# Kernel optimization log

Measured on AMD Instinct MI355X. Metric: run time of the kernel, lower is better.

## Reference

```python
import jax, jax.numpy as jnp
import numpy as np

N, C_IN, C_OUT, W_DIM, H, W = 16, 512, 512, 512, 64, 64

def setup_inputs() -> dict:
    key = jax.random.key(0)
    ks = jax.random.split(key, 6)
    return {
        "x": jax.random.normal(ks[0], (N, C_IN, H, W), dtype=jnp.float32),
        "w": jax.random.normal(ks[1], (N, W_DIM), dtype=jnp.float32),
        "noise": jax.random.normal(ks[2], (N, 1, H, W), dtype=jnp.float32),
        "affine_w": jax.random.normal(ks[3], (C_IN, W_DIM), dtype=jnp.float32) * (1.0 / np.sqrt(W_DIM)),
        "affine_b": jnp.ones((C_IN,), dtype=jnp.float32),  # bias_init=1.0
        "noise_strength": jnp.ones((), dtype=jnp.float32),
        "conv_w": jax.random.normal(ks[4], (C_OUT, C_IN, 3, 3), dtype=jnp.float32),
        "conv_b": jnp.zeros((C_OUT,), dtype=jnp.float32),
    }

def reference(x, w, noise, affine_w, affine_b, noise_strength, conv_w, conv_b):
    # affine: s = w @ affine_w.T + affine_b  (no activation)
    s = jnp.einsum('nd,cd->nc', w, affine_w) + affine_b  # [N, C_in]
    # Demodulated per-sample conv. Original builds w_n = W * s_n then demodulates;
    # since conv is linear in the weight's input-channel scale, this is equivalent to
    # scaling the input by s and the output by the demod factor d.
    w2 = jnp.sum(conv_w * conv_w, axis=(2, 3))  # [O, I]: sum over kernel taps
    d = jax.lax.rsqrt(jnp.einsum('ni,oi->no', s * s, w2) + 1e-8)  # [N, O]
    x_mod = x * s[:, :, None, None]
    y = jax.lax.conv_general_dilated(
        x_mod, conv_w, window_strides=(1, 1), padding='SAME',
        dimension_numbers=('NCHW', 'OIHW', 'NCHW'))  # [N, O, H, W]
    y = y * d[:, :, None, None] + conv_b[None, :, None, None]
    y = y + noise * noise_strength
    return jnp.where(y >= 0, y, 0.2 * y)  # LeakyReLU(0.2)
```

## Files before the change

kernel.cpp:

```cpp
#include <hip/hip_runtime.h>
#include <hip/hip_bf16.h>

typedef unsigned short u16;
typedef short bf16x8 __attribute__((ext_vector_type(8)));
typedef float f32x4 __attribute__((ext_vector_type(4)));

#define N_    16
#define CIN   512
#define COUT  512
#define WD    512
#define P_    4096
#define CC    (COUT * CIN)

#define OFF_S   0u
#define OFF_D   32768u
#define OFF_Z   65536u
#define OFF_WBT 131072u
#define OFF_XB  8388608u
#define WS_NEED (OFF_XB + 67108864u)

__device__ __forceinline__ u16 f2bf(float f) {
  union { float f; unsigned u; } a; a.f = f;
  unsigned r = a.u + 0x7fffu + ((a.u >> 16) & 1u);
  return (u16)(r >> 16);
}

__device__ __forceinline__ void gl_lds16(const u16* g, u16* l) {
  __builtin_amdgcn_global_load_lds(
      (const __attribute__((address_space(1))) void*)g,
      (__attribute__((address_space(3))) void*)l, 16, 0, 0);
}

__global__ void k_zero(float* z) { z[threadIdx.x] = 0.f; }

__global__ __launch_bounds__(256) void k_affine(const float* __restrict__ w,
                                                const float* __restrict__ aw,
                                                const float* __restrict__ ab,
                                                float* __restrict__ s) {
  int idx = blockIdx.x * 256 + threadIdx.x;
  int n = idx >> 9, c = idx & 511;
  const float4* wr = (const float4*)(w + (size_t)n * WD);
  const float4* ar = (const float4*)(aw + (size_t)c * WD);
  float acc = 0.f;
#pragma unroll 4
  for (int k = 0; k < WD / 4; ++k) {
    float4 a = wr[k], b = ar[k];
    acc += a.x * b.x + a.y * b.y + a.z * b.z + a.w * b.w;
  }
  s[idx] = acc + ab[c];
}

__global__ __launch_bounds__(256) void k_demod(const float* __restrict__ s,
                                               const float* __restrict__ cw,
                                               float* __restrict__ d) {
  __shared__ float w2[CIN];
  int o = blockIdx.x;
  const float* wr = cw + (size_t)o * CIN * 9;
  for (int i = threadIdx.x; i < CIN; i += 256) {
    float acc = 0.f;
#pragma unroll
    for (int t = 0; t < 9; ++t) { float v = wr[i * 9 + t]; acc += v * v; }
    w2[i] = acc;
  }
  __syncthreads();
  int wave = threadIdx.x >> 6, lane = threadIdx.x & 63;
  for (int nn = wave; nn < N_; nn += 4) {
    float acc = 0.f;
    for (int i = lane; i < CIN; i += 64) {
      float sv = s[nn * CIN + i];
      acc += sv * sv * w2[i];
    }
#pragma unroll
    for (int off = 32; off > 0; off >>= 1) acc += __shfl_down(acc, off);
    if (lane == 0) {
      float a = acc + 1e-8f;
      float r = rsqrtf(a);
      r = r * (1.5f - 0.5f * a * r * r);
      d[nn * COUT + o] = r;
    }
  }
}

__global__ __launch_bounds__(256) void k_wprep(const float* __restrict__ cw,
                                               u16* __restrict__ wbt) {
  int idx = blockIdx.x * 256 + threadIdx.x;
  if (idx >= COUT * CIN * 9) return;
  int t = idx % 9; int oi = idx / 9; int i = oi & 511; int o = oi >> 9;
  wbt[((size_t)t * COUT + o) * CIN + i] = f2bf(cw[idx]);
}

__global__ __launch_bounds__(256) void k_xmod(const float* __restrict__ x,
                                              const float* __restrict__ s,
                                              u16* __restrict__ xb) {
  __shared__ float tile[64][65];
  int b = blockIdx.x;
  int pt = b & 63; int ct = (b >> 6) & 7; int n = b >> 9;
  int c0 = ct * 64, p0 = pt * 64;
  const float* xp = x + ((size_t)n * CIN + c0) * P_ + p0;
  int t = threadIdx.x;
#pragma unroll
  for (int pass = 0; pass < 4; ++pass) {
    int r = pass * 16 + (t >> 4);
    int col4 = (t & 15);
    float4 v = *(const float4*)(xp + (size_t)r * P_ + col4 * 4);
    float sc = s[n * CIN + c0 + r];
    tile[r][col4 * 4 + 0] = v.x * sc;
    tile[r][col4 * 4 + 1] = v.y * sc;
    tile[r][col4 * 4 + 2] = v.z * sc;
    tile[r][col4 * 4 + 3] = v.w * sc;
  }
  __syncthreads();
  int p = t >> 2, cq = (t & 3) * 16;
  union { u16 us[16]; uint4 q[2]; } pk;
#pragma unroll
  for (int j = 0; j < 16; ++j) pk.us[j] = f2bf(tile[cq + j][p]);
  uint4* dst = (uint4*)(xb + ((size_t)n * P_ + p0 + p) * CIN + c0 + cq);
  dst[0] = pk.q[0];
  dst[1] = pk.q[1];
}

__global__ __launch_bounds__(256, 2) void k_conv(const u16* __restrict__ xb,
                                                 const u16* __restrict__ wbt,
                                                 const u16* __restrict__ zp,
                                                 const float* __restrict__ dmod,
                                                 const float* __restrict__ cbias,
                                                 const float* __restrict__ noise,
                                                 const float* __restrict__ nstr,
                                                 float* __restrict__ out) {
  __shared__ u16 smA[3][8192];
  __shared__ u16 smB[3][4096];

  int bid = blockIdx.x;
  int wg = (bid & 7) * 128 + (bid >> 3);
  int n = wg >> 6;
  int rem = wg & 63;
  int ob = rem >> 5;
  int pb = rem & 31;

  int tid = threadIdx.x;
  int wv = tid >> 6, l = tid & 63;
  int wr = wv >> 1, wc = wv & 1;
  int lrow = l & 15, kgrp = l >> 4;
  int prs = kgrp ^ ((lrow >> 1) & 3);

  int rowbase = (wv << 4) + (l >> 2);
  int kslot = (l & 3) ^ ((l >> 3) & 3);
  const u16* xbn = xb + (size_t)n * P_ * CIN;

  const u16* baseA = wbt + (size_t)(ob * 256 + rowbase) * CIN + kslot * 8;

  auto bsrc_for_tap = [&](int tapn, int c) -> const u16* {
    int dh = tapn < 3 ? -1 : (tapn < 6 ? 0 : 1);
    int dw = tapn - (dh + 1) * 3 - 1;
    int hh = pb * 2 + c + dh, ww = rowbase + dw;
    bool val = ((unsigned)hh < 64u) && ((unsigned)ww < 64u);
    return val ? (xbn + ((size_t)((hh << 6) + ww)) * CIN + kslot * 8)
               : (zp + kslot * 8);
  };

  auto stage_A = [&](int tt, int buf) {
    int tapn = tt >> 4, cbn = tt & 15;
    const u16* p = baseA + (size_t)tapn * CC + cbn * 32;
#pragma unroll
    for (int c = 0; c < 4; ++c)
      gl_lds16(p + c * 64 * CIN, &smA[buf][c * 2048 + wv * 512]);
  };
  auto stage_B = [&](int tt, int buf) {
    int tapn = tt >> 4, cbn = tt & 15;
#pragma unroll
    for (int c = 0; c < 2; ++c)
      gl_lds16(bsrc_for_tap(tapn, c) + cbn * 32, &smB[buf][c * 2048 + wv * 512]);
  };

  f32x4 acc0[4][4], acc1[4][4];
  f32x4 zero = {0.f, 0.f, 0.f, 0.f};
#pragma unroll
  for (int i = 0; i < 4; ++i)
#pragma unroll
    for (int j = 0; j < 4; ++j) { acc0[i][j] = zero; acc1[i][j] = zero; }

  stage_A(0, 0); stage_B(0, 0);
  stage_A(1, 1); stage_B(1, 1);

  int tap3 = 0, cb3 = 2;
  const u16* rpA = baseA + 2 * 32;
  const u16* rpB[2];
#pragma unroll
  for (int c = 0; c < 2; ++c) rpB[c] = bsrc_for_tap(0, c) + 2 * 32;

  int bcur = 0, bstg = 2;
  for (int t = 0; t < 144; ++t) {
    if (t <= 142) asm volatile("s_waitcnt vmcnt(6)" ::: "memory");
    else          asm volatile("s_waitcnt vmcnt(0)" ::: "memory");
    __builtin_amdgcn_s_barrier();
    __builtin_amdgcn_sched_barrier(0);

    const u16* A = smA[bcur];
    const u16* B = smB[bcur];

    bf16x8 Bf[4], Af0[4], Af1[4];
#pragma unroll
    for (int ni = 0; ni < 4; ++ni)
      Bf[ni] = *(const bf16x8*)&B[(wc * 64 + ni * 16 + lrow) * 32 + prs * 8];
#pragma unroll
    for (int mi = 0; mi < 4; ++mi)
      Af0[mi] = *(const bf16x8*)&A[(wr * 128 + mi * 16 + lrow) * 32 + prs * 8];
    __builtin_amdgcn_sched_barrier(0);
#pragma unroll
    for (int mi = 0; mi < 4; ++mi)
      Af1[mi] = *(const bf16x8*)&A[(wr * 128 + 64 + mi * 16 + lrow) * 32 + prs * 8];

    if (t <= 141) {
#pragma unroll
      for (int c = 0; c < 4; ++c)
        gl_lds16(rpA + c * 64 * CIN, &smA[bstg][c * 2048 + wv * 512]);
#pragma unroll
      for (int c = 0; c < 2; ++c)
        gl_lds16(rpB[c], &smB[bstg][c * 2048 + wv * 512]);
      cb3++;
      if (cb3 == 16) {
        cb3 = 0; tap3++;
        rpA = baseA + (size_t)tap3 * CC;
#pragma unroll
        for (int c = 0; c < 2; ++c) rpB[c] = bsrc_for_tap(tap3, c);
      } else {
        rpA += 32;
#pragma unroll
        for (int c = 0; c < 2; ++c) rpB[c] += 32;
      }
    }

    asm volatile("s_waitcnt lgkmcnt(4)" ::: "memory");
    __builtin_amdgcn_sched_barrier(0);
    __builtin_amdgcn_s_setprio(1);
#pragma unroll
    for (int mi = 0; mi < 4; ++mi)
#pragma unroll
      for (int ni = 0; ni < 4; ++ni)
        acc0[mi][ni] = __builtin_amdgcn_mfma_f32_16x16x32_bf16(
            Af0[mi], Bf[ni], acc0[mi][ni], 0, 0, 0);
    __builtin_amdgcn_s_setprio(0);

    asm volatile("s_waitcnt lgkmcnt(0)" ::: "memory");
    __builtin_amdgcn_sched_barrier(0);
    __builtin_amdgcn_s_setprio(1);
#pragma unroll
    for (int mi = 0; mi < 4; ++mi)
#pragma unroll
      for (int ni = 0; ni < 4; ++ni)
        acc1[mi][ni] = __builtin_amdgcn_mfma_f32_16x16x32_bf16(
            Af1[mi], Bf[ni], acc1[mi][ni], 0, 0, 0);
    __builtin_amdgcn_s_setprio(0);

    bcur = (bcur == 2) ? 0 : bcur + 1;
    bstg = (bstg == 2) ? 0 : bstg + 1;
  }

  float ns = nstr[0];
  const float* noise_n = noise + (size_t)n * P_;
  float nz[4];
#pragma unroll
  for (int ni = 0; ni < 4; ++ni)
    nz[ni] = noise_n[pb * 128 + wc * 64 + ni * 16 + lrow] * ns;

  auto epi = [&](f32x4 (&A_)[4][4], int qm) {
#pragma unroll
    for (int mi = 0; mi < 4; ++mi) {
      int o0 = ob * 256 + wr * 128 + qm * 64 + mi * 16 + kgrp * 4;
#pragma unroll
      for (int r = 0; r < 4; ++r) {
        int o = o0 + r;
        float dv = dmod[n * COUT + o];
        float bv = cbias[o];
        float* orow = out + ((size_t)(n * COUT + o)) * P_ + pb * 128 + wc * 64;
#pragma unroll
        for (int ni = 0; ni < 4; ++ni) {
          float v = A_[mi][ni][r] * dv + bv + nz[ni];
          orow[ni * 16 + lrow] = v >= 0.f ? v : 0.2f * v;
        }
      }
    }
  };
  epi(acc0, 0);
  epi(acc1, 1);
}

__global__ __launch_bounds__(64) void k_conv_naive(const float* __restrict__ x,
                                                   const float* __restrict__ cw,
                                                   const float* __restrict__ cbias,
                                                   const float* __restrict__ noise,
                                                   const float* __restrict__ nstr,
                                                   const float* __restrict__ s,
                                                   const float* __restrict__ d,
                                                   float* __restrict__ out) {
  int bid = blockIdx.x;
  int h = bid & 63; int o = (bid >> 6) & 511; int n = bid >> 15;
  int wcol = threadIdx.x;
  float acc = 0.f;
  for (int i = 0; i < CIN; ++i) {
    float sv = s[n * CIN + i];
    const float* xrow = x + ((size_t)(n * CIN + i)) * P_;
    const float* wrp = cw + ((size_t)o * CIN + i) * 9;
#pragma unroll
    for (int t = 0; t < 9; ++t) {
      int hh = h + t / 3 - 1, ww = wcol + t % 3 - 1;
      float xv = ((unsigned)hh < 64u && (unsigned)ww < 64u) ? xrow[hh * 64 + ww] : 0.f;
      acc += xv * sv * wrp[t];
    }
  }
  float v = acc * d[n * COUT + o] + cbias[o] + noise[(size_t)n * P_ + h * 64 + wcol] * nstr[0];
  out[((size_t)(n * COUT + o)) * P_ + h * 64 + wcol] = v >= 0.f ? v : 0.2f * v;
}

extern "C" void kernel_launch(void* const* d_in, const int* in_sizes, int n_in,
                              void* d_out, int out_size, void* d_ws, size_t ws_size,
                              hipStream_t stream) {
  const float* x    = (const float*)d_in[0];
  const float* w    = (const float*)d_in[1];
  const float* noise= (const float*)d_in[2];
  const float* aw   = (const float*)d_in[3];
  const float* ab   = (const float*)d_in[4];
  const float* nstr = (const float*)d_in[5];
  const float* cw   = (const float*)d_in[6];
  const float* cb   = (const float*)d_in[7];
  float* out = (float*)d_out;
  char* ws = (char*)d_ws;
  float* s = (float*)(ws + OFF_S);
  float* d = (float*)(ws + OFF_D);

  k_affine<<<(N_ * COUT) / 256, 256, 0, stream>>>(w, aw, ab, s);
  k_demod<<<COUT, 256, 0, stream>>>(s, cw, d);

  if (ws_size >= WS_NEED) {
    u16* zp  = (u16*)(ws + OFF_Z);
    u16* wbt = (u16*)(ws + OFF_WBT);
    u16* xbb = (u16*)(ws + OFF_XB);
    k_zero<<<1, 256, 0, stream>>>((float*)zp);
    k_wprep<<<(COUT * CIN * 9 + 255) / 256, 256, 0, stream>>>(cw, wbt);
    k_xmod<<<N_ * 8 * 64, 256, 0, stream>>>(x, s, xbb);
    k_conv<<<1024, 256, 0, stream>>>(xbb, wbt, zp, d, cb, noise, nstr, out);
  } else {
    k_conv_naive<<<N_ * COUT * 64, 64, 0, stream>>>(x, cw, cb, noise, nstr, s, d, out);
  }
}
```

Measured before the change: 358.7 us.

## Enlarge conv block tile to 256x256 with 8x8 MFMA accumulators per wave

Doubles the pixel dimension of each workgroup's output tile from 128 to 256 (four image rows), so each wave holds an 8x8 grid of 16x16 accumulators and the grid shrinks to 512 blocks. This raises arithmetic intensity by reusing each loaded weight tile over twice as many pixels, cutting global/LDS traffic per FLOP. In exchange, register use roughly doubles (256 accumulator VGPRs), occupancy drops to one block per CU, LDS grows, and 512 blocks on 256 CUs leaves less latency hiding and possible tail effects.

```diff
diff --git a/kernel.cpp b/kernel.cpp
--- a/kernel.cpp
+++ b/kernel.cpp
@@ -119,7 +119,7 @@
   dst[1] = pk.q[1];
 }
 
-__global__ __launch_bounds__(256, 2) void k_conv(const u16* __restrict__ xb,
+__global__ __launch_bounds__(256, 1) void k_conv(const u16* __restrict__ xb,
                                                  const u16* __restrict__ wbt,
                                                  const u16* __restrict__ zp,
                                                  const float* __restrict__ dmod,
@@ -128,14 +128,14 @@
                                                  const float* __restrict__ nstr,
                                                  float* __restrict__ out) {
   __shared__ u16 smA[3][8192];
-  __shared__ u16 smB[3][4096];
+  __shared__ u16 smB[3][8192];
 
   int bid = blockIdx.x;
-  int wg = (bid & 7) * 128 + (bid >> 3);
-  int n = wg >> 6;
-  int rem = wg & 63;
-  int ob = rem >> 5;
-  int pb = rem & 31;
+  int wg = (bid & 7) * 64 + (bid >> 3);
+  int n = wg >> 5;
+  int rem = wg & 31;
+  int ob = rem >> 4;
+  int pb = rem & 15;
 
   int tid = threadIdx.x;
   int wv = tid >> 6, l = tid & 63;
@@ -143,54 +143,57 @@
   int lrow = l & 15, kgrp = l >> 4;
   int prs = kgrp ^ ((lrow >> 1) & 3);
 
-  int rowbase = (wv << 4) + (l >> 2);
-  int kslot = (l & 3) ^ ((l >> 3) & 3);
+  int srl = l >> 2;
+  int lslot = (l & 3) ^ ((l >> 3) & 3);
   const u16* xbn = xb + (size_t)n * P_ * CIN;
 
-  const u16* baseA = wbt + (size_t)(ob * 256 + rowbase) * CIN + kslot * 8;
-
-  auto bsrc_for_tap = [&](int tapn, int c) -> const u16* {
+  int hgj[4], wgj[4];
+#pragma unroll
+  for (int j = 0; j < 4; ++j) {
+    int rB = wv * 64 + j * 16 + srl;
+    hgj[j] = pb * 4 + (rB >> 6);
+    wgj[j] = rB & 63;
+  }
+  const u16* srcA_base[4];
+#pragma unroll
+  for (int j = 0; j < 4; ++j)
+    srcA_base[j] = wbt + (size_t)(ob * 256 + wv * 64 + j * 16 + srl) * CIN + lslot * 8;
+
+  auto bsrc_for_tap = [&](int tapn, int j) -> const u16* {
     int dh = tapn < 3 ? -1 : (tapn < 6 ? 0 : 1);
     int dw = tapn - (dh + 1) * 3 - 1;
-    int hh = pb * 2 + c + dh, ww = rowbase + dw;
+    int hh = hgj[j] + dh, ww = wgj[j] + dw;
     bool val = ((unsigned)hh < 64u) && ((unsigned)ww < 64u);
-    return val ? (xbn + ((size_t)((hh << 6) + ww)) * CIN + kslot * 8)
-               : (zp + kslot * 8);
+    return val ? (xbn + ((size_t)((hh << 6) + ww)) * CIN + lslot * 8)
+               : (zp + lslot * 8);
   };
 
-  auto stage_A = [&](int tt, int buf) {
-    int tapn = tt >> 4, cbn = tt & 15;
-    const u16* p = baseA + (size_t)tapn * CC + cbn * 32;
-#pragma unroll
-    for (int c = 0; c < 4; ++c)
-      gl_lds16(p + c * 64 * CIN, &smA[buf][c * 2048 + wv * 512]);
-  };
-  auto stage_B = [&](int tt, int buf) {
-    int tapn = tt >> 4, cbn = tt & 15;
-#pragma unroll
-    for (int c = 0; c < 2; ++c)
-      gl_lds16(bsrc_for_tap(tapn, c) + cbn * 32, &smB[buf][c * 2048 + wv * 512]);
-  };
-
-  f32x4 acc0[4][4], acc1[4][4];
+  f32x4 acc[8][8];
   f32x4 zero = {0.f, 0.f, 0.f, 0.f};
 #pragma unroll
-  for (int i = 0; i < 4; ++i)
-#pragma unroll
-    for (int j = 0; j < 4; ++j) { acc0[i][j] = zero; acc1[i][j] = zero; }
-
-  stage_A(0, 0); stage_B(0, 0);
-  stage_A(1, 1); stage_B(1, 1);
+  for (int i = 0; i < 8; ++i)
+#pragma unroll
+    for (int j = 0; j < 8; ++j) acc[i][j] = zero;
+
+#pragma unroll
+  for (int tt = 0; tt < 2; ++tt) {
+#pragma unroll
+    for (int j = 0; j < 4; ++j)
+      gl_lds16(srcA_base[j] + tt * 32, &smA[tt][(wv * 64 + j * 16) * 32]);
+#pragma unroll
+    for (int j = 0; j < 4; ++j)
+      gl_lds16(bsrc_for_tap(0, j) + tt * 32, &smB[tt][(wv * 64 + j * 16) * 32]);
+  }
 
   int tap3 = 0, cb3 = 2;
-  const u16* rpA = baseA + 2 * 32;
-  const u16* rpB[2];
-#pragma unroll
-  for (int c = 0; c < 2; ++c) rpB[c] = bsrc_for_tap(0, c) + 2 * 32;
+  int aoff = 2 * 32;
+  const u16* rpB[4];
+#pragma unroll
+  for (int j = 0; j < 4; ++j) rpB[j] = bsrc_for_tap(0, j) + 2 * 32;
 
   int bcur = 0, bstg = 2;
   for (int t = 0; t < 144; ++t) {
-    if (t <= 142) asm volatile("s_waitcnt vmcnt(6)" ::: "memory");
+    if (t <= 142) asm volatile("s_waitcnt vmcnt(8)" ::: "memory");
     else          asm volatile("s_waitcnt vmcnt(0)" ::: "memory");
     __builtin_amdgcn_s_barrier();
     __builtin_amdgcn_sched_barrier(0);
@@ -198,37 +201,39 @@
     const u16* A = smA[bcur];
     const u16* B = smB[bcur];
 
-    bf16x8 Bf[4], Af0[4], Af1[4];
-#pragma unroll
-    for (int ni = 0; ni < 4; ++ni)
-      Bf[ni] = *(const bf16x8*)&B[(wc * 64 + ni * 16 + lrow) * 32 + prs * 8];
+    bf16x8 Bf[8], Af[8];
+#pragma unroll
+    for (int ni = 0; ni < 8; ++ni)
+      Bf[ni] = *(const bf16x8*)&B[(wc * 128 + ni * 16 + lrow) * 32 + prs * 8];
 #pragma unroll
     for (int mi = 0; mi < 4; ++mi)
-      Af0[mi] = *(const bf16x8*)&A[(wr * 128 + mi * 16 + lrow) * 32 + prs * 8];
-    __builtin_amdgcn_sched_barrier(0);
-#pragma unroll
-    for (int mi = 0; mi < 4; ++mi)
-      Af1[mi] = *(const bf16x8*)&A[(wr * 128 + 64 + mi * 16 + lrow) * 32 + prs * 8];
+      Af[mi] = *(const bf16x8*)&A[(wr * 128 + mi * 16 + lrow) * 32 + prs * 8];
+    __builtin_amdgcn_sched_barrier(0);
+#pragma unroll
+    for (int mi = 4; mi < 8; ++mi)
+      Af[mi] = *(const bf16x8*)&A[(wr * 128 + mi * 16 + lrow) * 32 + prs * 8];
+    __builtin_amdgcn_sched_barrier(0);
 
     if (t <= 141) {
 #pragma unroll
-      for (int c = 0; c < 4; ++c)
-        gl_lds16(rpA + c * 64 * CIN, &smA[bstg][c * 2048 + wv * 512]);
-#pragma unroll
-      for (int c = 0; c < 2; ++c)
-        gl_lds16(rpB[c], &smB[bstg][c * 2048 + wv * 512]);
+      for (int j = 0; j < 4; ++j)
+        gl_lds16(srcA_base[j] + aoff, &smA[bstg][(wv * 64 + j * 16) * 32]);
+#pragma unroll
+      for (int j = 0; j < 4; ++j)
+        gl_lds16(rpB[j], &smB[bstg][(wv * 64 + j * 16) * 32]);
       cb3++;
       if (cb3 == 16) {
         cb3 = 0; tap3++;
-        rpA = baseA + (size_t)tap3 * CC;
-#pragma unroll
-        for (int c = 0; c < 2; ++c) rpB[c] = bsrc_for_tap(tap3, c);
+        aoff = tap3 * CC;
+#pragma unroll
+        for (int j = 0; j < 4; ++j) rpB[j] = bsrc_for_tap(tap3, j);
       } else {
-        rpA += 32;
-#pragma unroll
-        for (int c = 0; c < 2; ++c) rpB[c] += 32;
+        aoff += 32;
+#pragma unroll
+        for (int j = 0; j < 4; ++j) rpB[j] += 32;
       }
     }
+    __builtin_amdgcn_sched_barrier(0);
 
     asm volatile("s_waitcnt lgkmcnt(4)" ::: "memory");
     __builtin_amdgcn_sched_barrier(0);
@@ -236,20 +241,20 @@
 #pragma unroll
     for (int mi = 0; mi < 4; ++mi)
 #pragma unroll
-      for (int ni = 0; ni < 4; ++ni)
-        acc0[mi][ni] = __builtin_amdgcn_mfma_f32_16x16x32_bf16(
-            Af0[mi], Bf[ni], acc0[mi][ni], 0, 0, 0);
+      for (int ni = 0; ni < 8; ++ni)
+        acc[mi][ni] = __builtin_amdgcn_mfma_f32_16x16x32_bf16(
+            Af[mi], Bf[ni], acc[mi][ni], 0, 0, 0);
     __builtin_amdgcn_s_setprio(0);
 
     asm volatile("s_waitcnt lgkmcnt(0)" ::: "memory");
     __builtin_amdgcn_sched_barrier(0);
     __builtin_amdgcn_s_setprio(1);
 #pragma unroll
-    for (int mi = 0; mi < 4; ++mi)
-#pragma unroll
-      for (int ni = 0; ni < 4; ++ni)
-        acc1[mi][ni] = __builtin_amdgcn_mfma_f32_16x16x32_bf16(
-            Af1[mi], Bf[ni], acc1[mi][ni], 0, 0, 0);
+    for (int mi = 4; mi < 8; ++mi)
+#pragma unroll
+      for (int ni = 0; ni < 8; ++ni)
+        acc[mi][ni] = __builtin_amdgcn_mfma_f32_16x16x32_bf16(
+            Af[mi], Bf[ni], acc[mi][ni], 0, 0, 0);
     __builtin_amdgcn_s_setprio(0);
 
     bcur = (bcur == 2) ? 0 : bcur + 1;
@@ -258,31 +263,27 @@
 
   float ns = nstr[0];
   const float* noise_n = noise + (size_t)n * P_;
-  float nz[4];
-#pragma unroll
-  for (int ni = 0; ni < 4; ++ni)
-    nz[ni] = noise_n[pb * 128 + wc * 64 + ni * 16 + lrow] * ns;
-
-  auto epi = [&](f32x4 (&A_)[4][4], int qm) {
-#pragma unroll
-    for (int mi = 0; mi < 4; ++mi) {
-      int o0 = ob * 256 + wr * 128 + qm * 64 + mi * 16 + kgrp * 4;
-#pragma unroll
-      for (int r = 0; r < 4; ++r) {
-        int o = o0 + r;
-        float dv = dmod[n * COUT + o];
-        float bv = cbias[o];
-        float* orow = out + ((size_t)(n * COUT + o)) * P_ + pb * 128 + wc * 64;
-#pragma unroll
-        for (int ni = 0; ni < 4; ++ni) {
-          float v = A_[mi][ni][r] * dv + bv + nz[ni];
-          orow[ni * 16 + lrow] = v >= 0.f ? v : 0.2f * v;
-        }
+  float nz[8];
+#pragma unroll
+  for (int ni = 0; ni < 8; ++ni)
+    nz[ni] = noise_n[pb * 256 + wc * 128 + ni * 16 + lrow] * ns;
+
+#pragma unroll
+  for (int mi = 0; mi < 8; ++mi) {
+    int o0 = ob * 256 + wr * 128 + mi * 16 + kgrp * 4;
+#pragma unroll
+    for (int r = 0; r < 4; ++r) {
+      int o = o0 + r;
+      float dv = dmod[n * COUT + o];
+      float bv = cbias[o];
+      float* orow = out + ((size_t)(n * COUT + o)) * P_ + pb * 256 + wc * 128;
+#pragma unroll
+      for (int ni = 0; ni < 8; ++ni) {
+        float v = acc[mi][ni][r] * dv + bv + nz[ni];
+        orow[ni * 16 + lrow] = v >= 0.f ? v : 0.2f * v;
       }
     }
-  };
-  epi(acc0, 0);
-  epi(acc1, 1);
+  }
 }
 
 __global__ __launch_bounds__(64) void k_conv_naive(const float* __restrict__ x,
@@ -338,7 +339,7 @@
     k_zero<<<1, 256, 0, stream>>>((float*)zp);
     k_wprep<<<(COUT * CIN * 9 + 255) / 256, 256, 0, stream>>>(cw, wbt);
     k_xmod<<<N_ * 8 * 64, 256, 0, stream>>>(x, s, xbb);
-    k_conv<<<1024, 256, 0, stream>>>(xbb, wbt, zp, d, cb, noise, nstr, out);
+    k_conv<<<512, 256, 0, stream>>>(xbb, wbt, zp, d, cb, noise, nstr, out);
   } else {
     k_conv_naive<<<N_ * COUT * 64, 64, 0, stream>>>(x, cw, cb, noise, nstr, s, d, out);
   }
```

After: 348.9 us. 2.7% less time.
